# Optimization experiments

Measured on AMD Instinct MI355X. Metric: run time of the kernel, lower is better.

Reference implementation:

```python
import jax, jax.numpy as jnp
import numpy as np

B, A = 4096, 8          # episodes, agents per episode
N = B * A               # total nodes
E = B * A * (A - 1)     # fully-connected directed edges within each group
F_IN, D, H, M, NA = 64, 64, 4, 64, 10  # in_feat, gnn_dim, heads, mem_dim, n_actions
NEG_SLOPE = 0.2
LN_EPS = 1e-5


def _build_edge_index():
    base = np.arange(A)
    s = np.repeat(base, A)
    d = np.tile(base, A)
    keep = s != d
    s, d = s[keep], d[keep]                       # [A*(A-1)]
    offs = (np.arange(B) * A)[:, None]
    src = (offs + s[None, :]).reshape(-1)
    dst = (offs + d[None, :]).reshape(-1)
    return jnp.asarray(np.stack([src, dst]), dtype=jnp.int32)  # [2, E]


def setup_inputs() -> dict:
    key = jax.random.key(0)
    ks = jax.random.split(key, 16)
    sc = 0.05
    return {
        "x": jax.random.normal(ks[0], (N, F_IN), jnp.float32),
        "edge_attr": jax.random.normal(ks[1], (E, 3), jnp.float32),
        "hidden": jax.random.normal(ks[2], (N, M), jnp.float32) * sc,
        "edge_index": _build_edge_index(),
        # GATv2 params
        "Wl": jax.random.normal(ks[3], (H * D, F_IN), jnp.float32) * sc,
        "bl": jnp.zeros((H * D,), jnp.float32),
        "Wr": jax.random.normal(ks[4], (H * D, F_IN), jnp.float32) * sc,
        "br": jnp.zeros((H * D,), jnp.float32),
        "We": jax.random.normal(ks[5], (H * D, 3), jnp.float32) * sc,
        "be": jnp.zeros((H * D,), jnp.float32),
        "att": jax.random.normal(ks[6], (H, D), jnp.float32) * sc,
        "bias_g": jnp.zeros((D,), jnp.float32),
        # GRUCell params (gate order r,z,n as in torch)
        "W_ih": jax.random.normal(ks[7], (3 * M, D), jnp.float32) * sc,
        "W_hh": jax.random.normal(ks[8], (3 * M, M), jnp.float32) * sc,
        "b_ih": jnp.zeros((3 * M,), jnp.float32),
        "b_hh": jnp.zeros((3 * M,), jnp.float32),
        # LayerNorm + output Linear
        "ln_g": jnp.ones((M,), jnp.float32),
        "ln_b": jnp.zeros((M,), jnp.float32),
        "Wq": jax.random.normal(ks[9], (NA, M), jnp.float32) * sc,
        "bq": jnp.zeros((NA,), jnp.float32),
    }


def reference(x, edge_attr, hidden, edge_index, Wl, bl, Wr, br, We, be, att,
              bias_g, W_ih, W_hh, b_ih, b_hh, ln_g, ln_b, Wq, bq):
    src, dst = edge_index[0], edge_index[1]
    # GATv2Conv (concat=False -> mean over heads), share_weights=False
    xl = (x @ Wl.T + bl).reshape(N, H, D)          # source projection
    xr = (x @ Wr.T + br).reshape(N, H, D)          # target projection
    ee = (edge_attr @ We.T + be).reshape(E, H, D)  # edge embedding
    m = jax.nn.leaky_relu(xl[src] + xr[dst] + ee, NEG_SLOPE)  # [E,H,D]
    logits = jnp.einsum('ehd,hd->eh', m, att)                  # [E,H]
    lmax = jax.ops.segment_max(logits, dst, num_segments=N)    # [N,H]
    ex = jnp.exp(logits - lmax[dst])
    denom = jax.ops.segment_sum(ex, dst, num_segments=N)       # [N,H]
    alpha = ex / denom[dst]                                    # softmax per target
    agg = jax.ops.segment_sum(alpha[:, :, None] * xl[src], dst, num_segments=N)  # [N,H,D]
    h_gnn = jax.nn.relu(agg.mean(axis=1) + bias_g)             # [N,D]
    # GRUCell
    gi = h_gnn @ W_ih.T + b_ih
    gh = hidden @ W_hh.T + b_hh
    ir, iz, inn = jnp.split(gi, 3, axis=-1)
    hr, hz, hn = jnp.split(gh, 3, axis=-1)
    r = jax.nn.sigmoid(ir + hr)
    z = jax.nn.sigmoid(iz + hz)
    n = jnp.tanh(inn + r * hn)
    h = (1.0 - z) * n + z * hidden                              # [N,M]
    # LayerNorm + Linear head
    mu = h.mean(axis=-1, keepdims=True)
    var = ((h - mu) ** 2).mean(axis=-1, keepdims=True)
    hln = (h - mu) / jnp.sqrt(var + LN_EPS) * ln_g + ln_b
    q = hln @ Wq.T + bq                                         # [N,NA]
    return q, h
```

## Files before the change

kernel.cpp:

```cpp
#include <hip/hip_runtime.h>

typedef unsigned short u16;
typedef unsigned int u32;
typedef __attribute__((ext_vector_type(8))) short bf16x8;
typedef __attribute__((ext_vector_type(4))) float f32x4;
typedef _Float16 f16;
typedef __attribute__((ext_vector_type(2))) f16 h2;
typedef __attribute__((ext_vector_type(8))) f16 h8;

#define NAG 8
#define EPB 4
#define NAGB 32
#define FIN 64
#define MDIM 64
#define NACT 10
#define EPG 56
#define NTOT 32768
#define ABP 72
#define XLS 296
#define XHS 72

#define U_XR  9472
#define U_RZ  0
#define U_HNH 8448
#define U_INB 10624
#define U_HG  12800
#define U_LNH 12800

#define WQOFF 57344

__device__ __forceinline__ float b2f(u16 u) {
  return __uint_as_float(((unsigned int)u) << 16);
}
__device__ __forceinline__ u16 f2b(float f) {
  unsigned int x = __float_as_uint(f);
  unsigned int r = x + 0x7fffu + ((x >> 16) & 1u);
  return (u16)(r >> 16);
}
__device__ __forceinline__ u16 f2h(float f) {
  f16 h = (f16)f; u16 u; __builtin_memcpy(&u, &h, 2); return u;
}
__device__ __forceinline__ float h2f(u16 u) {
  f16 h; __builtin_memcpy(&h, &u, 2); return (float)h;
}
__device__ __forceinline__ u32 pkh2(float a, float b) {
#if __has_builtin(__builtin_amdgcn_cvt_pkrtz)
  auto r = __builtin_amdgcn_cvt_pkrtz(a, b);
  u32 u; __builtin_memcpy(&u, &r, 4); return u;
#else
  return (u32)f2h(a) | ((u32)f2h(b) << 16);
#endif
}

union H8u { h8 v; h2 p[4]; };

__device__ __forceinline__ h8 lrelu8(h8 m) {
  h8 s = m * (f16)0.2f;
#if __has_builtin(__builtin_elementwise_max)
  return __builtin_elementwise_max(m, s);
#else
  h8 r;
#pragma unroll
  for (int i = 0; i < 8; i++) r[i] = (m[i] > s[i]) ? m[i] : s[i];
  return r;
#endif
}

#if __has_builtin(__builtin_amdgcn_fdot2)
__device__ __forceinline__ float dotacc(h2 a, h2 b, float c) {
  return __builtin_amdgcn_fdot2(a, b, c, false);
}
#else
__device__ __forceinline__ float dotacc(h2 a, h2 b, float c) {
  c += (float)a[0] * (float)b[0];
  c += (float)a[1] * (float)b[1];
  return c;
}
#endif

__global__ __launch_bounds__(256) void prep_weights(
    const float* __restrict__ Wl, const float* __restrict__ Wr,
    const float* __restrict__ Wih, const float* __restrict__ Whh,
    const float* __restrict__ Wq,
    u16* __restrict__ wsB)
{
  const int idx = blockIdx.x * 256 + threadIdx.x;
  if (idx >= 57 * 2 * 64) return;
  const int L  = idx & 63;
  const int ks = (idx >> 6) & 1;
  const int T  = idx >> 7;
  u16 v[8];
  if (T < 56) {
    const float* W; int row0;
    if      (T < 16) { W = Wl;  row0 = T * 16; }
    else if (T < 32) { W = Wr;  row0 = (T - 16) * 16; }
    else if (T < 44) { W = Wih; row0 = (T - 32) * 16; }
    else             { W = Whh; row0 = (T - 44) * 16; }
    const int row = row0 + (L & 15);
    const int k0  = ks * 32 + (L >> 4) * 8;
#pragma unroll
    for (int j = 0; j < 8; j++) v[j] = f2b(W[row * 64 + k0 + j]);
  } else {
    const int row = L & 15;
    const int k0  = ks * 32 + (L >> 4) * 8;
#pragma unroll
    for (int j = 0; j < 8; j++)
      v[j] = (row < NACT) ? f2h(Wq[row * 64 + k0 + j]) : (u16)0;
  }
  *(bf16x8*)(wsB + (size_t)idx * 8) = *(bf16x8*)v;
}

__global__ __launch_bounds__(512, 6) void gnn_rnn_kernel(
    const float* __restrict__ x, const float* __restrict__ edge_attr,
    const float* __restrict__ hidden,
    const float* __restrict__ bl, const float* __restrict__ br,
    const float* __restrict__ We, const float* __restrict__ be,
    const float* __restrict__ att, const float* __restrict__ bias_g,
    const float* __restrict__ b_ih, const float* __restrict__ b_hh,
    const float* __restrict__ ln_g, const float* __restrict__ ln_b,
    const float* __restrict__ Wq, const float* __restrict__ bq,
    const u16* __restrict__ wsB,
    float* __restrict__ d_out)
{
  __shared__ __align__(16) char uraw[37888];
  __shared__ __align__(16) u16 s_xb[NAGB * ABP];
  __shared__ __align__(16) u16 s_al[NAGB * 4 * 8];
  __shared__ __align__(16) u16 s_hidb[NAGB * ABP];
  __shared__ __align__(16) u16 s_w0h[256], s_w1h[256], s_w2h[256], s_atth[256];

  u16*   uXL  = (u16*)uraw;
  u16*   uXR  = (u16*)uraw + U_XR;
  u16*   uHn  = (u16*)uraw + U_HNH;
  u16*   uInn = (u16*)uraw + U_INB;
  u16*   s_hgb = (u16*)uraw + U_HG;
  u16*   uLnH = (u16*)uraw + U_LNH;
  float* uF   = (float*)uraw;

  const int t = threadIdx.x;
  const int b = blockIdx.x;
  const int L = t & 63;
  const int w = t >> 6;
  const int q = L >> 4;

  {
    const float4 xv = ((const float4*)(x + b * (NAGB * FIN)))[t];
    const float4 hv = ((const float4*)(hidden + b * (NAGB * MDIM)))[t];
    const int a = t >> 4, m = (t * 4) & 63;
    u16 px[4] = { f2b(xv.x), f2b(xv.y), f2b(xv.z), f2b(xv.w) };
    u16 ph[4] = { f2b(hv.x), f2b(hv.y), f2b(hv.z), f2b(hv.w) };
    *(uint2*)&s_xb[a * ABP + m]   = *(uint2*)px;
    *(uint2*)&s_hidb[a * ABP + m] = *(uint2*)ph;
    if (t < 256) {
      s_w0h[t]  = f2h(We[t * 3]);
      s_w1h[t]  = f2h(We[t * 3 + 1]);
      s_w2h[t]  = f2h(We[t * 3 + 2]);
      s_atth[t] = f2h(att[t]);
    }
  }
  const int h3 = w >> 1, epa = w & 1;
  float eaA0 = 0.f, eaA1 = 0.f, eaA2 = 0.f, eaB0 = 0.f, eaB1 = 0.f, eaB2 = 0.f;
  if (L < EPG) {
    const float* eb = edge_attr + b * (EPB * EPG * 3) + epa * (EPG * 3) + L * 3;
    eaA0 = eb[0]; eaA1 = eb[1]; eaA2 = eb[2];
    eaB0 = eb[2 * EPG * 3]; eaB1 = eb[2 * EPG * 3 + 1]; eaB2 = eb[2 * EPG * 3 + 2];
  }
  __syncthreads();

  {
    const int g = w & 1;
    const int arow = g * 16 + (L & 15);
    bf16x8 af0 = *(const bf16x8*)&s_xb[arow * ABP + q * 8];
    bf16x8 af1 = *(const bf16x8*)&s_xb[arow * ABP + 32 + q * 8];
    const bf16x8* wsBv = (const bf16x8*)wsB;
#pragma unroll
    for (int i = 0; i < 8; i++) {
      const int T = (w >> 1) * 8 + i;
      f32x4 acc = {0.f, 0.f, 0.f, 0.f};
      acc = __builtin_amdgcn_mfma_f32_16x16x32_bf16(wsBv[(T * 2 + 0) * 64 + L], af0, acc, 0, 0, 0);
      acc = __builtin_amdgcn_mfma_f32_16x16x32_bf16(wsBv[(T * 2 + 1) * 64 + L], af1, acc, 0, 0, 0);
      const int Tm = T & 15;
      const int h = Tm >> 2;
      const int gcb = Tm * 16 + q * 4;
      const int d0 = (Tm & 3) * 16 + q * 4;
      f32x4 bias4;
      if (T < 16) bias4 = *(const f32x4*)(bl + gcb);
      else        bias4 = *(const f32x4*)(br + gcb) + *(const f32x4*)(be + gcb);
      f32x4 v = acc + bias4;
      u32 pk2[2] = { pkh2(v[0], v[1]), pkh2(v[2], v[3]) };
      u16* dst = (T < 16 ? uXL : uXR) + arow * XLS + h * XHS + d0;
      *(uint2*)dst = *(uint2*)pk2;
    }
  }
  __syncthreads();

  {
    if (L < EPG) {
      const int e = L;
      const int s = e / 7, k = e % 7;
      const int j = k + (k >= s ? 1 : 0);
      const f16 a00 = (f16)eaA0, a01 = (f16)eaA1, a02 = (f16)eaA2;
      const f16 a10 = (f16)eaB0, a11 = (f16)eaB1, a12 = (f16)eaB2;
      const int epA = epa, epB = epa + 2;
      const u16* xlp0 = uXL + (epA * 8 + s) * XLS + h3 * XHS;
      const u16* xrp0 = uXR + (epA * 8 + j) * XLS + h3 * XHS;
      const u16* xlp1 = uXL + (epB * 8 + s) * XLS + h3 * XHS;
      const u16* xrp1 = uXR + (epB * 8 + j) * XLS + h3 * XHS;
      const u16* w0p = s_w0h + h3 * 64;
      const u16* w1p = s_w1h + h3 * 64;
      const u16* w2p = s_w2h + h3 * 64;
      const u16* atp = s_atth + h3 * 64;
      float lgA0 = 0.f, lgB0 = 0.f, lgA1 = 0.f, lgB1 = 0.f;
#pragma unroll 2
      for (int kq = 0; kq < 8; kq++) {
        H8u w0, w1, w2, at, x0, r0, x1, r1, m0, m1;
        w0.v = *(const h8*)(w0p + kq * 8);
        w1.v = *(const h8*)(w1p + kq * 8);
        w2.v = *(const h8*)(w2p + kq * 8);
        at.v = *(const h8*)(atp + kq * 8);
        x0.v = *(const h8*)(xlp0 + kq * 8);
        r0.v = *(const h8*)(xrp0 + kq * 8);
        x1.v = *(const h8*)(xlp1 + kq * 8);
        r1.v = *(const h8*)(xrp1 + kq * 8);
        m0.v = x0.v + r0.v + w0.v * a00 + w1.v * a01 + w2.v * a02;
        m0.v = lrelu8(m0.v);
        m1.v = x1.v + r1.v + w0.v * a10 + w1.v * a11 + w2.v * a12;
        m1.v = lrelu8(m1.v);
        lgA0 = dotacc(m0.p[0], at.p[0], lgA0);
        lgB0 = dotacc(m0.p[1], at.p[1], lgB0);
        lgA0 = dotacc(m0.p[2], at.p[2], lgA0);
        lgB0 = dotacc(m0.p[3], at.p[3], lgB0);
        lgA1 = dotacc(m1.p[0], at.p[0], lgA1);
        lgB1 = dotacc(m1.p[1], at.p[1], lgB1);
        lgA1 = dotacc(m1.p[2], at.p[2], lgA1);
        lgB1 = dotacc(m1.p[3], at.p[3], lgB1);
      }
      s_al[((epa * 8 + j) * 4 + h3) * 8 + s]       = f2h(__expf(lgA0 + lgB0));
      s_al[(((epa + 2) * 8 + j) * 4 + h3) * 8 + s] = f2h(__expf(lgA1 + lgB1));
    } else {
      const int j2 = L - EPG;
      s_al[((epa * 8 + j2) * 4 + h3) * 8 + j2]       = 0;
      s_al[(((epa + 2) * 8 + j2) * 4 + h3) * 8 + j2] = 0;
    }
  }
  __syncthreads();

  {
    const int ep = t >> 7, jj = (t >> 4) & 7, dq = t & 15;
    const int a32 = ep * 8 + jj;
    float acc[4] = {0.f, 0.f, 0.f, 0.f};
#pragma unroll
    for (int h = 0; h < 4; h++) {
      H8u av;
      av.v = *(const h8*)&s_al[(a32 * 4 + h) * 8];
      h2 d2 = (av.p[0] + av.p[1]) + (av.p[2] + av.p[3]);
      float den = (float)d2[0] + (float)d2[1];
      h2 ah0 = {(f16)0.f, (f16)0.f};
      h2 ah1 = {(f16)0.f, (f16)0.f};
#pragma unroll
      for (int s = 0; s < 8; s++) {
        const u16* xp = uXL + (ep * 8 + s) * XLS + h * XHS + dq * 4;
        uint2 xv = *(const uint2*)xp;
        h2 x01, x23;
        __builtin_memcpy(&x01, &xv.x, 4);
        __builtin_memcpy(&x23, &xv.y, 4);
        f16 al = av.v[s];
        h2 al2 = {al, al};
        ah0 += al2 * x01;
        ah1 += al2 * x23;
      }
      const float inv = 1.f / den;
      acc[0] += (float)ah0[0] * inv;
      acc[1] += (float)ah0[1] * inv;
      acc[2] += (float)ah1[0] * inv;
      acc[3] += (float)ah1[1] * inv;
    }
    const f32x4 bg = *(const f32x4*)(bias_g + dq * 4);
    u16 pk[4];
#pragma unroll
    for (int c = 0; c < 4; c++) {
      float v = acc[c] * 0.25f + bg[c];
      pk[c] = f2b(v > 0.f ? v : 0.f);
    }
    *(uint2*)&s_hgb[a32 * ABP + dq * 4] = *(uint2*)pk;
  }
  __syncthreads();

  {
    const int g = w & 1;
    const int arow = g * 16 + (L & 15);
    bf16x8 ag0 = *(const bf16x8*)&s_hgb[arow * ABP + q * 8];
    bf16x8 ag1 = *(const bf16x8*)&s_hgb[arow * ABP + 32 + q * 8];
    bf16x8 ah0 = *(const bf16x8*)&s_hidb[arow * ABP + q * 8];
    bf16x8 ah1 = *(const bf16x8*)&s_hidb[arow * ABP + 32 + q * 8];
    const bf16x8* wsBv = (const bf16x8*)wsB;
#pragma unroll
    for (int i = 0; i < 3; i++) {
      const int T6 = (w >> 1) * 3 + i;
      const int Tg = 32 + T6, Th = 44 + T6;
      f32x4 acci = {0.f, 0.f, 0.f, 0.f};
      acci = __builtin_amdgcn_mfma_f32_16x16x32_bf16(wsBv[(Tg * 2 + 0) * 64 + L], ag0, acci, 0, 0, 0);
      acci = __builtin_amdgcn_mfma_f32_16x16x32_bf16(wsBv[(Tg * 2 + 1) * 64 + L], ag1, acci, 0, 0, 0);
      f32x4 acch = {0.f, 0.f, 0.f, 0.f};
      acch = __builtin_amdgcn_mfma_f32_16x16x32_bf16(wsBv[(Th * 2 + 0) * 64 + L], ah0, acch, 0, 0, 0);
      acch = __builtin_amdgcn_mfma_f32_16x16x32_bf16(wsBv[(Th * 2 + 1) * 64 + L], ah1, acch, 0, 0, 0);
      const int gcb = T6 * 16 + q * 4;
      if (T6 < 8) {
        f32x4 bsum = *(const f32x4*)(b_ih + gcb) + *(const f32x4*)(b_hh + gcb);
        f32x4 v = acci + acch + bsum;
        *(f32x4*)&uF[U_RZ + arow * 132 + gcb] = v;
      } else {
        f32x4 vi = acci + *(const f32x4*)(b_ih + gcb);
        f32x4 vh = acch + *(const f32x4*)(b_hh + gcb);
        const int off = arow * 68 + (gcb - 128);
        u32 pi[2] = { pkh2(vi[0], vi[1]), pkh2(vi[2], vi[3]) };
        u32 ph[2] = { pkh2(vh[0], vh[1]), pkh2(vh[2], vh[3]) };
        *(uint2*)&uInn[off] = *(uint2*)pi;
        *(uint2*)&uHn[off]  = *(uint2*)ph;
      }
    }
  }
  __syncthreads();

  {
    const float lng = ln_g[L];
    const float lnb = ln_b[L];
#pragma unroll
    for (int rr = 0; rr < 4; rr++) {
      const int a = w + rr * 8, m = L;
      float rz_r = uF[U_RZ + a * 132 + m];
      float rz_z = uF[U_RZ + a * 132 + 64 + m];
      float inn  = h2f(uInn[a * 68 + m]);
      float hn   = h2f(uHn[a * 68 + m]);
      float hid  = b2f(s_hidb[a * ABP + m]);
      float r = 1.f / (1.f + __expf(-rz_r));
      float z = 1.f / (1.f + __expf(-rz_z));
      float xg = inn + r * hn;
      xg = fminf(fmaxf(xg, -20.f), 20.f);
      float e2 = __expf(2.f * xg);
      float n = (e2 - 1.f) / (e2 + 1.f);
      float hv = (1.f - z) * n + z * hid;
      d_out[NTOT * NACT + (b * NAGB + a) * MDIM + m] = hv;
      float sum = hv, sq = hv * hv;
#pragma unroll
      for (int off = 1; off < 64; off <<= 1) {
        sum += __shfl_xor(sum, off, 64);
        sq  += __shfl_xor(sq,  off, 64);
      }
      float mu  = sum * (1.f / 64.f);
      float var = sq * (1.f / 64.f) - mu * mu;
      var = var > 0.f ? var : 0.f;
      uLnH[a * ABP + m] = f2h((hv - mu) * rsqrtf(var + 1e-5f) * lng + lnb);
    }
  }
  __syncthreads();

  if (w < 2) {
    const int agent = w * 16 + (L & 15);
    const u16* wq = wsB + WQOFF;
    h8 wq0, wq1, ln0, ln1;
    wq0 = *(const h8*)(wq + (size_t)(0 * 64 + L) * 8);
    wq1 = *(const h8*)(wq + (size_t)(1 * 64 + L) * 8);
    ln0 = *(const h8*)(uLnH + agent * ABP + q * 8);
    ln1 = *(const h8*)(uLnH + agent * ABP + 32 + q * 8);
    f32x4 acc = {0.f, 0.f, 0.f, 0.f};
    acc = __builtin_amdgcn_mfma_f32_16x16x32_f16(wq0, ln0, acc, 0, 0, 0);
    acc = __builtin_amdgcn_mfma_f32_16x16x32_f16(wq1, ln1, acc, 0, 0, 0);
    float* qout = d_out + ((size_t)b * NAGB + agent) * NACT;
#pragma unroll
    for (int r = 0; r < 4; r++) {
      const int o = q * 4 + r;
      if (o < NACT) qout[o] = acc[r] + bq[o];
    }
  }
}

extern "C" void kernel_launch(void* const* d_in, const int* in_sizes, int n_in,
                              void* d_out, int out_size, void* d_ws, size_t ws_size,
                              hipStream_t stream) {
  const int N  = in_sizes[0] / FIN;
  const int Bn = N / NAGB;
  u16* wsB = (u16*)d_ws;

  prep_weights<<<29, 256, 0, stream>>>(
      (const float*)d_in[4],
      (const float*)d_in[6],
      (const float*)d_in[12],
      (const float*)d_in[13],
      (const float*)d_in[18],
      wsB);

  gnn_rnn_kernel<<<Bn, 512, 0, stream>>>(
      (const float*)d_in[0], (const float*)d_in[1], (const float*)d_in[2],
      (const float*)d_in[5],
      (const float*)d_in[7],
      (const float*)d_in[8],
      (const float*)d_in[9],
      (const float*)d_in[10],
      (const float*)d_in[11],
      (const float*)d_in[14],
      (const float*)d_in[15],
      (const float*)d_in[16], (const float*)d_in[17],
      (const float*)d_in[18], (const float*)d_in[19],
      wsB, (float*)d_out);
}
```

Measured before the change: 133.2 us.

## Drop weight prep kernel; load fp32 weights in-kernel and use f16 MFMA

Removes the separate prep_weights launch that pre-swizzled weights into bf16 MFMA fragments in workspace. Each block now loads the fp32 Wl/Wr/W_ih/W_hh/Wq rows directly and packs them to f16 in registers, so the MFMA paths switch from bf16 to f16 and the activation staging also moves to f16. This saves one kernel launch and the workspace round trip. In exchange every block repeats the fp32 weight loads and conversions (relying on L2 hits), loop unrolling is reduced, and f16's narrower range may affect precision.

```diff
diff --git a/kernel.cpp b/kernel.cpp
--- a/kernel.cpp
+++ b/kernel.cpp
@@ -2,7 +2,6 @@
 
 typedef unsigned short u16;
 typedef unsigned int u32;
-typedef __attribute__((ext_vector_type(8))) short bf16x8;
 typedef __attribute__((ext_vector_type(4))) float f32x4;
 typedef _Float16 f16;
 typedef __attribute__((ext_vector_type(2))) f16 h2;
@@ -27,16 +26,6 @@
 #define U_HG  12800
 #define U_LNH 12800
 
-#define WQOFF 57344
-
-__device__ __forceinline__ float b2f(u16 u) {
-  return __uint_as_float(((unsigned int)u) << 16);
-}
-__device__ __forceinline__ u16 f2b(float f) {
-  unsigned int x = __float_as_uint(f);
-  unsigned int r = x + 0x7fffu + ((x >> 16) & 1u);
-  return (u16)(r >> 16);
-}
 __device__ __forceinline__ u16 f2h(float f) {
   f16 h = (f16)f; u16 u; __builtin_memcpy(&u, &h, 2); return u;
 }
@@ -51,6 +40,12 @@
   return (u32)f2h(a) | ((u32)f2h(b) << 16);
 #endif
 }
+__device__ __forceinline__ h8 ld8h(const float* __restrict__ p) {
+  f32x4 a = *(const f32x4*)p;
+  f32x4 b = *(const f32x4*)(p + 4);
+  u32 v[4] = { pkh2(a[0], a[1]), pkh2(a[2], a[3]), pkh2(b[0], b[1]), pkh2(b[2], b[3]) };
+  h8 r; __builtin_memcpy(&r, v, 16); return r;
+}
 
 union H8u { h8 v; h2 p[4]; };
 
@@ -78,48 +73,17 @@
 }
 #endif
 
-__global__ __launch_bounds__(256) void prep_weights(
-    const float* __restrict__ Wl, const float* __restrict__ Wr,
-    const float* __restrict__ Wih, const float* __restrict__ Whh,
-    const float* __restrict__ Wq,
-    u16* __restrict__ wsB)
-{
-  const int idx = blockIdx.x * 256 + threadIdx.x;
-  if (idx >= 57 * 2 * 64) return;
-  const int L  = idx & 63;
-  const int ks = (idx >> 6) & 1;
-  const int T  = idx >> 7;
-  u16 v[8];
-  if (T < 56) {
-    const float* W; int row0;
-    if      (T < 16) { W = Wl;  row0 = T * 16; }
-    else if (T < 32) { W = Wr;  row0 = (T - 16) * 16; }
-    else if (T < 44) { W = Wih; row0 = (T - 32) * 16; }
-    else             { W = Whh; row0 = (T - 44) * 16; }
-    const int row = row0 + (L & 15);
-    const int k0  = ks * 32 + (L >> 4) * 8;
-#pragma unroll
-    for (int j = 0; j < 8; j++) v[j] = f2b(W[row * 64 + k0 + j]);
-  } else {
-    const int row = L & 15;
-    const int k0  = ks * 32 + (L >> 4) * 8;
-#pragma unroll
-    for (int j = 0; j < 8; j++)
-      v[j] = (row < NACT) ? f2h(Wq[row * 64 + k0 + j]) : (u16)0;
-  }
-  *(bf16x8*)(wsB + (size_t)idx * 8) = *(bf16x8*)v;
-}
-
 __global__ __launch_bounds__(512, 6) void gnn_rnn_kernel(
     const float* __restrict__ x, const float* __restrict__ edge_attr,
     const float* __restrict__ hidden,
+    const float* __restrict__ Wl, const float* __restrict__ Wr,
+    const float* __restrict__ W_ih, const float* __restrict__ W_hh,
     const float* __restrict__ bl, const float* __restrict__ br,
     const float* __restrict__ We, const float* __restrict__ be,
     const float* __restrict__ att, const float* __restrict__ bias_g,
     const float* __restrict__ b_ih, const float* __restrict__ b_hh,
     const float* __restrict__ ln_g, const float* __restrict__ ln_b,
     const float* __restrict__ Wq, const float* __restrict__ bq,
-    const u16* __restrict__ wsB,
     float* __restrict__ d_out)
 {
   __shared__ __align__(16) char uraw[37888];
@@ -141,13 +105,15 @@
   const int L = t & 63;
   const int w = t >> 6;
   const int q = L >> 4;
+  const int wrow = L & 15;
+  const int kc = (L >> 4) * 8;
 
   {
     const float4 xv = ((const float4*)(x + b * (NAGB * FIN)))[t];
     const float4 hv = ((const float4*)(hidden + b * (NAGB * MDIM)))[t];
     const int a = t >> 4, m = (t * 4) & 63;
-    u16 px[4] = { f2b(xv.x), f2b(xv.y), f2b(xv.z), f2b(xv.w) };
-    u16 ph[4] = { f2b(hv.x), f2b(hv.y), f2b(hv.z), f2b(hv.w) };
+    u32 px[2] = { pkh2(xv.x, xv.y), pkh2(xv.z, xv.w) };
+    u32 ph[2] = { pkh2(hv.x, hv.y), pkh2(hv.z, hv.w) };
     *(uint2*)&s_xb[a * ABP + m]   = *(uint2*)px;
     *(uint2*)&s_hidb[a * ABP + m] = *(uint2*)ph;
     if (t < 256) {
@@ -168,16 +134,19 @@
 
   {
     const int g = w & 1;
-    const int arow = g * 16 + (L & 15);
-    bf16x8 af0 = *(const bf16x8*)&s_xb[arow * ABP + q * 8];
-    bf16x8 af1 = *(const bf16x8*)&s_xb[arow * ABP + 32 + q * 8];
-    const bf16x8* wsBv = (const bf16x8*)wsB;
-#pragma unroll
+    const int arow = g * 16 + wrow;
+    h8 af0 = *(const h8*)&s_xb[arow * ABP + q * 8];
+    h8 af1 = *(const h8*)&s_xb[arow * ABP + 32 + q * 8];
+#pragma unroll 2
     for (int i = 0; i < 8; i++) {
       const int T = (w >> 1) * 8 + i;
+      const float* Wp = (T < 16) ? (Wl + (T * 16 + wrow) * 64)
+                                 : (Wr + ((T - 16) * 16 + wrow) * 64);
+      h8 wf0 = ld8h(Wp + kc);
+      h8 wf1 = ld8h(Wp + 32 + kc);
       f32x4 acc = {0.f, 0.f, 0.f, 0.f};
-      acc = __builtin_amdgcn_mfma_f32_16x16x32_bf16(wsBv[(T * 2 + 0) * 64 + L], af0, acc, 0, 0, 0);
-      acc = __builtin_amdgcn_mfma_f32_16x16x32_bf16(wsBv[(T * 2 + 1) * 64 + L], af1, acc, 0, 0, 0);
+      acc = __builtin_amdgcn_mfma_f32_16x16x32_f16(wf0, af0, acc, 0, 0, 0);
+      acc = __builtin_amdgcn_mfma_f32_16x16x32_f16(wf1, af1, acc, 0, 0, 0);
       const int Tm = T & 15;
       const int h = Tm >> 2;
       const int gcb = Tm * 16 + q * 4;
@@ -275,34 +244,38 @@
       acc[3] += (float)ah1[1] * inv;
     }
     const f32x4 bg = *(const f32x4*)(bias_g + dq * 4);
-    u16 pk[4];
-#pragma unroll
-    for (int c = 0; c < 4; c++) {
-      float v = acc[c] * 0.25f + bg[c];
-      pk[c] = f2b(v > 0.f ? v : 0.f);
-    }
-    *(uint2*)&s_hgb[a32 * ABP + dq * 4] = *(uint2*)pk;
+    float v0 = acc[0] * 0.25f + bg[0];
+    float v1 = acc[1] * 0.25f + bg[1];
+    float v2 = acc[2] * 0.25f + bg[2];
+    float v3 = acc[3] * 0.25f + bg[3];
+    u32 pk2[2] = { pkh2(v0 > 0.f ? v0 : 0.f, v1 > 0.f ? v1 : 0.f),
+                   pkh2(v2 > 0.f ? v2 : 0.f, v3 > 0.f ? v3 : 0.f) };
+    *(uint2*)&s_hgb[a32 * ABP + dq * 4] = *(uint2*)pk2;
   }
   __syncthreads();
 
   {
     const int g = w & 1;
-    const int arow = g * 16 + (L & 15);
-    bf16x8 ag0 = *(const bf16x8*)&s_hgb[arow * ABP + q * 8];
-    bf16x8 ag1 = *(const bf16x8*)&s_hgb[arow * ABP + 32 + q * 8];
-    bf16x8 ah0 = *(const bf16x8*)&s_hidb[arow * ABP + q * 8];
-    bf16x8 ah1 = *(const bf16x8*)&s_hidb[arow * ABP + 32 + q * 8];
-    const bf16x8* wsBv = (const bf16x8*)wsB;
-#pragma unroll
+    const int arow = g * 16 + wrow;
+    h8 ag0 = *(const h8*)&s_hgb[arow * ABP + q * 8];
+    h8 ag1 = *(const h8*)&s_hgb[arow * ABP + 32 + q * 8];
+    h8 ah0 = *(const h8*)&s_hidb[arow * ABP + q * 8];
+    h8 ah1 = *(const h8*)&s_hidb[arow * ABP + 32 + q * 8];
+#pragma unroll 1
     for (int i = 0; i < 3; i++) {
       const int T6 = (w >> 1) * 3 + i;
-      const int Tg = 32 + T6, Th = 44 + T6;
+      const float* Wip = W_ih + (T6 * 16 + wrow) * 64;
+      const float* Whp = W_hh + (T6 * 16 + wrow) * 64;
+      h8 wi0 = ld8h(Wip + kc);
+      h8 wi1 = ld8h(Wip + 32 + kc);
+      h8 wh0 = ld8h(Whp + kc);
+      h8 wh1 = ld8h(Whp + 32 + kc);
       f32x4 acci = {0.f, 0.f, 0.f, 0.f};
-      acci = __builtin_amdgcn_mfma_f32_16x16x32_bf16(wsBv[(Tg * 2 + 0) * 64 + L], ag0, acci, 0, 0, 0);
-      acci = __builtin_amdgcn_mfma_f32_16x16x32_bf16(wsBv[(Tg * 2 + 1) * 64 + L], ag1, acci, 0, 0, 0);
+      acci = __builtin_amdgcn_mfma_f32_16x16x32_f16(wi0, ag0, acci, 0, 0, 0);
+      acci = __builtin_amdgcn_mfma_f32_16x16x32_f16(wi1, ag1, acci, 0, 0, 0);
       f32x4 acch = {0.f, 0.f, 0.f, 0.f};
-      acch = __builtin_amdgcn_mfma_f32_16x16x32_bf16(wsBv[(Th * 2 + 0) * 64 + L], ah0, acch, 0, 0, 0);
-      acch = __builtin_amdgcn_mfma_f32_16x16x32_bf16(wsBv[(Th * 2 + 1) * 64 + L], ah1, acch, 0, 0, 0);
+      acch = __builtin_amdgcn_mfma_f32_16x16x32_f16(wh0, ah0, acch, 0, 0, 0);
+      acch = __builtin_amdgcn_mfma_f32_16x16x32_f16(wh1, ah1, acch, 0, 0, 0);
       const int gcb = T6 * 16 + q * 4;
       if (T6 < 8) {
         f32x4 bsum = *(const f32x4*)(b_ih + gcb) + *(const f32x4*)(b_hh + gcb);
@@ -331,7 +304,7 @@
       float rz_z = uF[U_RZ + a * 132 + 64 + m];
       float inn  = h2f(uInn[a * 68 + m]);
       float hn   = h2f(uHn[a * 68 + m]);
-      float hid  = b2f(s_hidb[a * ABP + m]);
+      float hid  = h2f(s_hidb[a * ABP + m]);
       float r = 1.f / (1.f + __expf(-rz_r));
       float z = 1.f / (1.f + __expf(-rz_z));
       float xg = inn + r * hn;
@@ -355,13 +328,15 @@
   __syncthreads();
 
   if (w < 2) {
-    const int agent = w * 16 + (L & 15);
-    const u16* wq = wsB + WQOFF;
-    h8 wq0, wq1, ln0, ln1;
-    wq0 = *(const h8*)(wq + (size_t)(0 * 64 + L) * 8);
-    wq1 = *(const h8*)(wq + (size_t)(1 * 64 + L) * 8);
-    ln0 = *(const h8*)(uLnH + agent * ABP + q * 8);
-    ln1 = *(const h8*)(uLnH + agent * ABP + 32 + q * 8);
+    const int agent = w * 16 + wrow;
+    h8 wq0 = {}, wq1 = {};
+    if (wrow < NACT) {
+      const float* Wqp = Wq + wrow * 64;
+      wq0 = ld8h(Wqp + kc);
+      wq1 = ld8h(Wqp + 32 + kc);
+    }
+    h8 ln0 = *(const h8*)(uLnH + agent * ABP + q * 8);
+    h8 ln1 = *(const h8*)(uLnH + agent * ABP + 32 + q * 8);
     f32x4 acc = {0.f, 0.f, 0.f, 0.f};
     acc = __builtin_amdgcn_mfma_f32_16x16x32_f16(wq0, ln0, acc, 0, 0, 0);
     acc = __builtin_amdgcn_mfma_f32_16x16x32_f16(wq1, ln1, acc, 0, 0, 0);
@@ -379,18 +354,14 @@
                               hipStream_t stream) {
   const int N  = in_sizes[0] / FIN;
   const int Bn = N / NAGB;
-  u16* wsB = (u16*)d_ws;
-
-  prep_weights<<<29, 256, 0, stream>>>(
+  (void)d_ws; (void)ws_size;
+
+  gnn_rnn_kernel<<<Bn, 512, 0, stream>>>(
+      (const float*)d_in[0], (const float*)d_in[1], (const float*)d_in[2],
       (const float*)d_in[4],
       (const float*)d_in[6],
       (const float*)d_in[12],
       (const float*)d_in[13],
-      (const float*)d_in[18],
-      wsB);
-
-  gnn_rnn_kernel<<<Bn, 512, 0, stream>>>(
-      (const float*)d_in[0], (const float*)d_in[1], (const float*)d_in[2],
       (const float*)d_in[5],
       (const float*)d_in[7],
       (const float*)d_in[8],
@@ -401,5 +372,5 @@
       (const float*)d_in[15],
       (const float*)d_in[16], (const float*)d_in[17],
       (const float*)d_in[18], (const float*)d_in[19],
-      wsB, (float*)d_out);
-}
+      (float*)d_out);
+}
```

Result: slower. 170.9 us (+28.4%).
